# Performance work log

Measured on AMD Instinct MI355X. Metric: run time of the kernel, lower is better.

## Reference

```python
import jax, jax.numpy as jnp
import numpy as np

K = 0.001  # sigmoid temperature from DGCLoss init
EPS = 1e-8


def _off_diag(m):
    # [..., n, n] -> [..., n, n-1], removing the diagonal in row-major order
    n = m.shape[-1]
    lead = m.shape[:-2]
    flat = m.reshape(lead + (n * n,))[..., :-1]
    return flat.reshape(lead + (n - 1, n + 1))[..., 1:].reshape(lead + (n, n - 1))


def setup_inputs() -> dict:
    key = jax.random.key(0)
    k1, k2 = jax.random.split(key)
    ranking = jax.random.normal(k1, (384, 256), dtype=jnp.float32)
    gt = jax.random.randint(k2, (384,), 0, 6, dtype=jnp.int64)
    return {"ranking": ranking, "gt": gt}


def reference(ranking, gt):
    x = ranking
    N = x.shape[0]
    # cosine similarity matrix, mapped to [0, 1]
    xn = x / jnp.clip(jnp.linalg.norm(x, axis=1, keepdims=True), EPS, None)
    sm = (xn @ xn.T + 1.0) * 0.5                         # [N, N]
    rank = _off_diag(sm)                                 # [N, N-1]
    g = jnp.abs(gt[None, :] - gt[:, None]).astype(jnp.float32)  # [N, N]
    g = _off_diag(g)                                     # [N, N-1]
    M = N - 1
    # dij[n, i, j] = rank[n, j] - rank[n, i]
    dij = rank[:, None, :] - rank[:, :, None]            # [N, M, M]
    dij = _off_diag(dij)                                 # [N, M, M-1]
    # clamped sigmoid indicator
    indicator = 1.0 / (1.0 + jnp.exp(jnp.clip(-dij / K, -50.0, 50.0)))
    indicator = indicator.sum(-1) + 1.0                  # [N, M]
    relevance = jnp.exp2(jnp.clip(10.0 - g, 0.0, None)) - 1.0  # [N, M]
    dcg = (relevance / jnp.log2(indicator + 1.0)).sum(axis=1)  # [N]
    # ideal DCG from sorted relevance
    rel_sorted = jnp.sort(relevance, axis=-1)[:, ::-1]
    discount = jnp.log2(jnp.arange(M, dtype=jnp.float32) + 2.0)
    idcg = (rel_sorted / discount).sum(axis=-1)          # [N]
    valid = idcg != 0.0
    ndcg = jnp.where(valid, dcg / jnp.where(valid, idcg, 1.0), 0.0)
    cnt = valid.sum()
    mean_ndcg = ndcg.sum() / jnp.maximum(cnt, 1).astype(jnp.float32)
    return jnp.where(cnt == 0, jnp.float32(1.0), 1.0 - mean_ndcg)
```

## Files before the change

### kernel.cpp

```cpp
#include <hip/hip_runtime.h>


#define NN 384
#define DD 256
#define MM 383
#define HSCALE 721.3475204444817f
#define NBUCK  256
#define BSCALE 0.1767955801104972f
#define WWIN   6.0f

__global__ __launch_bounds__(256) void dgc_normT(const float* __restrict__ x,
                                                 const int* __restrict__ gt,
                                                 float* __restrict__ XT,
                                                 float* __restrict__ XN,
                                                 float* __restrict__ idcg_tab) {
    const int t = threadIdx.x;

    if (blockIdx.x == 24) {
        __shared__ int   cnt[6];
        __shared__ int   cum[6][6];
        __shared__ float wred[4][6];
        const int lane = t & 63;
        const int wave = t >> 6;

        if (t < 6) cnt[t] = 0;
        __syncthreads();
        atomicAdd(&cnt[gt[t]], 1);
        if (t + 256 < NN) atomicAdd(&cnt[gt[t + 256]], 1);
        __syncthreads();
        if (t < 6) {
            int h[6];
            #pragma unroll
            for (int g = 0; g < 6; ++g) h[g] = 0;
            #pragma unroll
            for (int v = 0; v < 6; ++v) {
                int d = v - t; d = d < 0 ? -d : d;
                h[d] += cnt[v];
            }
            h[0] -= 1;
            int s = 0;
            #pragma unroll
            for (int g = 0; g < 6; ++g) { s += h[g]; cum[t][g] = s; }
        }
        __syncthreads();

        float acc[6] = {0.f, 0.f, 0.f, 0.f, 0.f, 0.f};
        for (int p = t; p < MM; p += 256) {
            const float invl = 1.0f / __builtin_amdgcn_logf((float)(p + 2));
            #pragma unroll
            for (int gv = 0; gv < 6; ++gv) {
                const int g = (p >= cum[gv][0]) + (p >= cum[gv][1])
                            + (p >= cum[gv][2]) + (p >= cum[gv][3])
                            + (p >= cum[gv][4]);
                acc[gv] += (float)((1 << (10 - g)) - 1) * invl;
            }
        }
        for (int off = 32; off > 0; off >>= 1) {
            #pragma unroll
            for (int gv = 0; gv < 6; ++gv) acc[gv] += __shfl_down(acc[gv], off, 64);
        }
        if (lane == 0) {
            #pragma unroll
            for (int gv = 0; gv < 6; ++gv) wred[wave][gv] = acc[gv];
        }
        __syncthreads();
        if (t < 6) idcg_tab[t] = wred[0][t] + wred[1][t] + wred[2][t] + wred[3][t];
        return;
    }

    __shared__ float xs[16][260];
    __shared__ float invn[16];
    const int r0 = blockIdx.x * 16;

    #pragma unroll
    for (int i = 0; i < 4; ++i) {
        int f = t + i * 256;
        int r = f >> 6, c4 = f & 63;
        float4 v = ((const float4*)(x + (size_t)(r0 + r) * DD))[c4];
        xs[r][c4 * 4 + 0] = v.x; xs[r][c4 * 4 + 1] = v.y;
        xs[r][c4 * 4 + 2] = v.z; xs[r][c4 * 4 + 3] = v.w;
    }
    __syncthreads();

    {
        const int r = t >> 4, sub = t & 15;
        float s = 0.0f;
        #pragma unroll
        for (int m = 0; m < 16; ++m) {
            float v = xs[r][sub * 16 + m];
            s = fmaf(v, v, s);
        }
        #pragma unroll
        for (int off = 8; off > 0; off >>= 1) s += __shfl_xor(s, off, 64);
        if (sub == 0) invn[r] = __builtin_amdgcn_rsqf(fmaxf(s, 1e-16f));
    }
    __syncthreads();

    {
        const int r  = t & 15;
        const int kk = t >> 4;
        const float inv = invn[r];
        #pragma unroll
        for (int i = 0; i < 16; ++i) {
            int k = i * 16 + kk;
            XT[(size_t)k * NN + r0 + r] = xs[r][k] * inv;
        }
    }
    {
        #pragma unroll
        for (int i = 0; i < 4; ++i) {
            int f = t + i * 256;
            int r = f >> 6, c4 = f & 63;
            const float inv = invn[r];
            float4 v;
            v.x = xs[r][c4 * 4 + 0] * inv; v.y = xs[r][c4 * 4 + 1] * inv;
            v.z = xs[r][c4 * 4 + 2] * inv; v.w = xs[r][c4 * 4 + 3] * inv;
            ((float4*)(XN + (size_t)(r0 + r) * DD))[c4] = v;
        }
    }
}

__global__ __launch_bounds__(768) void dgc_fused(const float* __restrict__ XT,
                                                 const float* __restrict__ XN,
                                                 const int* __restrict__ gt,
                                                 const float* __restrict__ idcg_tab,
                                                 float* __restrict__ ndcg) {
    __shared__ float  xs[2][DD];
    __shared__ float4 pacc[2][8][96];
    __shared__ float  srow[2][NN];
    __shared__ float  vsort[2][NN];
    __shared__ int    sidx[2][NN];
    __shared__ int    hist[2][NBUCK];
    __shared__ int    pre[2][NBUCK + 1];
    __shared__ float  redd[12];

    const int n0   = blockIdx.x * 2;
    const int t    = threadIdx.x;
    const int lane = t & 63;
    const int wave = t >> 6;

    if (t < 128)
        ((float4*)xs[t >> 6])[t & 63] =
            ((const float4*)(XN + (size_t)(n0 + (t >> 6)) * DD))[t & 63];
    if (t < 512) ((int*)hist)[t] = 0;
    __syncthreads();

    {
        const int j4 = t % 96;
        const int kc = t / 96;
        const float4* XT4 = (const float4*)XT;
        float4 a0 = {0.f, 0.f, 0.f, 0.f};
        float4 a1 = {0.f, 0.f, 0.f, 0.f};
        const int k0 = kc * 32;
        #pragma unroll 8
        for (int m = 0; m < 32; ++m) {
            const int k = k0 + m;
            float4 b = XT4[(size_t)k * 96 + j4];
            float s0 = xs[0][k];
            float s1 = xs[1][k];
            a0.x = fmaf(s0, b.x, a0.x); a0.y = fmaf(s0, b.y, a0.y);
            a0.z = fmaf(s0, b.z, a0.z); a0.w = fmaf(s0, b.w, a0.w);
            a1.x = fmaf(s1, b.x, a1.x); a1.y = fmaf(s1, b.y, a1.y);
            a1.z = fmaf(s1, b.z, a1.z); a1.w = fmaf(s1, b.w, a1.w);
        }
        pacc[0][kc][j4] = a0;
        pacc[1][kc][j4] = a1;
    }
    __syncthreads();

    const int r = t / 384;
    const int u = t - r * 384;

    {
        const float* pf = (const float*)pacc[r];
        float dot = 0.0f;
        #pragma unroll
        for (int c = 0; c < 8; ++c) dot += pf[c * 384 + u];
        srow[r][u] = fmaf(dot, HSCALE, HSCALE);
    }
    __syncthreads();

    const float vraw = srow[r][u];
    int b = (int)(vraw * BSCALE);
    b = b < 0 ? 0 : (b > NBUCK - 1 ? NBUCK - 1 : b);
    const int slot = atomicAdd(&hist[r][b], 1);
    __syncthreads();

    if (wave == 0 || wave == 6) {
        const int rr = wave / 6;
        const int s0 = hist[rr][lane * 4 + 0], s1 = hist[rr][lane * 4 + 1];
        const int s2 = hist[rr][lane * 4 + 2], s3 = hist[rr][lane * 4 + 3];
        const int sum = s0 + s1 + s2 + s3;
        int inc = sum;
        #pragma unroll
        for (int off = 1; off < 64; off <<= 1) {
            int uu = __shfl_up(inc, off, 64);
            if (lane >= off) inc += uu;
        }
        const int base = inc - sum;
        pre[rr][lane * 4 + 0] = base;
        pre[rr][lane * 4 + 1] = base + s0;
        pre[rr][lane * 4 + 2] = base + s0 + s1;
        pre[rr][lane * 4 + 3] = base + s0 + s1 + s2;
        if (lane == 63) pre[rr][NBUCK] = inc;
    }
    __syncthreads();

    {
        const int pos = pre[r][b] + slot;
        vsort[r][pos] = vraw;
        sidx[r][pos]  = u;
    }
    __syncthreads();

    const int   nrow  = n0 + r;
    const float ri    = vsort[r][u];
    const int   iorig = sidx[r][u];
    const float sn    = srow[r][nrow];

    int Blo = (int)((ri - WWIN) * BSCALE);
    int Bhi = (int)((ri + WWIN) * BSCALE);
    Blo = Blo < 0 ? 0 : (Blo > NBUCK - 1 ? NBUCK - 1 : Blo);
    Bhi = Bhi < 0 ? 0 : (Bhi > NBUCK - 1 ? NBUCK - 1 : Bhi);
    const int lo = pre[r][Blo];
    const int hi = pre[r][Bhi + 1];

    float p0 = 0.0f, p1 = 0.0f;
    int q = lo;
    for (; q + 2 <= hi; q += 2) {
        p0 += __builtin_amdgcn_rcpf(1.0f + __builtin_amdgcn_exp2f(ri - vsort[r][q]));
        p1 += __builtin_amdgcn_rcpf(1.0f + __builtin_amdgcn_exp2f(ri - vsort[r][q + 1]));
    }
    if (q < hi)
        p0 += __builtin_amdgcn_rcpf(1.0f + __builtin_amdgcn_exp2f(ri - vsort[r][q]));
    float sum_all = (float)(NN - hi) + p0 + p1;

    int bn = (int)(sn * BSCALE);
    bn = bn < 0 ? 0 : (bn > NBUCK - 1 ? NBUCK - 1 : bn);
    float cd = 0.0f;
    if (bn > Bhi)       cd = 1.0f;
    else if (bn >= Blo) cd = __builtin_amdgcn_rcpf(1.0f + __builtin_amdgcn_exp2f(ri - sn));
    const float ind = 0.5f + sum_all - cd;

    float dcg_i = 0.0f;
    if (iorig != nrow) {
        const int gd = gt[iorig] - gt[nrow];
        const int gg = gd < 0 ? -gd : gd;
        dcg_i = (float)((1 << (10 - gg)) - 1) / __builtin_amdgcn_logf(ind + 1.0f);
    }

    #pragma unroll
    for (int off = 32; off > 0; off >>= 1) dcg_i += __shfl_down(dcg_i, off, 64);
    if (lane == 0) redd[wave] = dcg_i;
    __syncthreads();
    if (t == 0)
        ndcg[n0] = (redd[0] + redd[1] + redd[2] + redd[3] + redd[4] + redd[5])
                   / idcg_tab[gt[n0]];
    if (t == 384)
        ndcg[n0 + 1] = (redd[6] + redd[7] + redd[8] + redd[9] + redd[10] + redd[11])
                       / idcg_tab[gt[n0 + 1]];
}

__global__ __launch_bounds__(384) void dgc_final(const float* __restrict__ ndcg,
                                                 float* __restrict__ out) {
    __shared__ float red[6];
    const int t    = threadIdx.x;
    const int lane = t & 63;
    const int wave = t >> 6;
    float nd = ndcg[t];
    #pragma unroll
    for (int off = 32; off > 0; off >>= 1) nd += __shfl_down(nd, off, 64);
    if (lane == 0) red[wave] = nd;
    __syncthreads();
    if (t == 0) {
        float s = 0.0f;
        for (int w = 0; w < 6; ++w) s += red[w];
        out[0] = 1.0f - s / (float)NN;
    }
}

extern "C" void kernel_launch(void* const* d_in, const int* in_sizes, int n_in,
                              void* d_out, int out_size, void* d_ws, size_t ws_size,
                              hipStream_t stream) {
    const float* ranking = (const float*)d_in[0];
    const int*   gt      = (const int*)d_in[1];
    float*       out     = (float*)d_out;

    float* XT   = (float*)d_ws;
    float* XN   = XT + (size_t)DD * NN;
    float* ndcg = XN + (size_t)NN * DD;
    float* tab  = ndcg + NN;

    dgc_normT<<<25, 256, 0, stream>>>(ranking, gt, XT, XN, tab);
    dgc_fused<<<NN / 2, 768, 0, stream>>>(XT, XN, gt, tab, ndcg);
    dgc_final<<<1, 384, 0, stream>>>(ndcg, out);
}
```

Before: 70.10 us.

## Drop final reduction kernel via atomic accumulation and pair sigmoid reciprocals

Removes the third kernel launch. The output is initialised to 1 in the first kernel, and each fused block atomically subtracts its normalised DCG contribution directly. Separately, the windowed sigmoid sum now combines two terms per reciprocal using 1/(1+a)+1/(1+b) = (2+a+b)/(1+a+b+ab), which halves the rcp count. In exchange, the float atomics make the summation order nondeterministic, and the product form can overflow to inf when both exponentials are large.

```diff
diff --git a/kernel.cpp b/kernel.cpp
--- a/kernel.cpp
+++ b/kernel.cpp
@@ -13,7 +13,8 @@
                                                  const int* __restrict__ gt,
                                                  float* __restrict__ XT,
                                                  float* __restrict__ XN,
-                                                 float* __restrict__ idcg_tab) {
+                                                 float* __restrict__ idcg_tab,
+                                                 float* __restrict__ out) {
     const int t = threadIdx.x;
 
     if (blockIdx.x == 24) {
@@ -23,6 +24,7 @@
         const int lane = t & 63;
         const int wave = t >> 6;
 
+        if (t == 0) out[0] = 1.0f;
         if (t < 6) cnt[t] = 0;
         __syncthreads();
         atomicAdd(&cnt[gt[t]], 1);
@@ -124,7 +126,7 @@
                                                  const float* __restrict__ XN,
                                                  const int* __restrict__ gt,
                                                  const float* __restrict__ idcg_tab,
-                                                 float* __restrict__ ndcg) {
+                                                 float* __restrict__ out) {
     __shared__ float  xs[2][DD];
     __shared__ float4 pacc[2][8][96];
     __shared__ float  srow[2][NN];
@@ -225,15 +227,18 @@
     const int lo = pre[r][Blo];
     const int hi = pre[r][Bhi + 1];
 
-    float p0 = 0.0f, p1 = 0.0f;
+    float acc = 0.0f;
     int q = lo;
     for (; q + 2 <= hi; q += 2) {
-        p0 += __builtin_amdgcn_rcpf(1.0f + __builtin_amdgcn_exp2f(ri - vsort[r][q]));
-        p1 += __builtin_amdgcn_rcpf(1.0f + __builtin_amdgcn_exp2f(ri - vsort[r][q + 1]));
+        float a = __builtin_amdgcn_exp2f(ri - vsort[r][q]);
+        float bb = __builtin_amdgcn_exp2f(ri - vsort[r][q + 1]);
+        float e = a + bb;
+        float f = a * bb;
+        acc = fmaf(2.0f + e, __builtin_amdgcn_rcpf(1.0f + e + f), acc);
     }
     if (q < hi)
-        p0 += __builtin_amdgcn_rcpf(1.0f + __builtin_amdgcn_exp2f(ri - vsort[r][q]));
-    float sum_all = (float)(NN - hi) + p0 + p1;
+        acc += __builtin_amdgcn_rcpf(1.0f + __builtin_amdgcn_exp2f(ri - vsort[r][q]));
+    float sum_all = (float)(NN - hi) + acc;
 
     int bn = (int)(sn * BSCALE);
     bn = bn < 0 ? 0 : (bn > NBUCK - 1 ? NBUCK - 1 : bn);
@@ -253,29 +258,13 @@
     for (int off = 32; off > 0; off >>= 1) dcg_i += __shfl_down(dcg_i, off, 64);
     if (lane == 0) redd[wave] = dcg_i;
     __syncthreads();
-    if (t == 0)
-        ndcg[n0] = (redd[0] + redd[1] + redd[2] + redd[3] + redd[4] + redd[5])
-                   / idcg_tab[gt[n0]];
-    if (t == 384)
-        ndcg[n0 + 1] = (redd[6] + redd[7] + redd[8] + redd[9] + redd[10] + redd[11])
-                       / idcg_tab[gt[n0 + 1]];
-}
-
-__global__ __launch_bounds__(384) void dgc_final(const float* __restrict__ ndcg,
-                                                 float* __restrict__ out) {
-    __shared__ float red[6];
-    const int t    = threadIdx.x;
-    const int lane = t & 63;
-    const int wave = t >> 6;
-    float nd = ndcg[t];
-    #pragma unroll
-    for (int off = 32; off > 0; off >>= 1) nd += __shfl_down(nd, off, 64);
-    if (lane == 0) red[wave] = nd;
-    __syncthreads();
     if (t == 0) {
-        float s = 0.0f;
-        for (int w = 0; w < 6; ++w) s += red[w];
-        out[0] = 1.0f - s / (float)NN;
+        float d = redd[0] + redd[1] + redd[2] + redd[3] + redd[4] + redd[5];
+        atomicAdd(out, -d / (idcg_tab[gt[n0]] * (float)NN));
+    }
+    if (t == 384) {
+        float d = redd[6] + redd[7] + redd[8] + redd[9] + redd[10] + redd[11];
+        atomicAdd(out, -d / (idcg_tab[gt[n0 + 1]] * (float)NN));
     }
 }
 
@@ -286,12 +275,10 @@
     const int*   gt      = (const int*)d_in[1];
     float*       out     = (float*)d_out;
 
-    float* XT   = (float*)d_ws;
-    float* XN   = XT + (size_t)DD * NN;
-    float* ndcg = XN + (size_t)NN * DD;
-    float* tab  = ndcg + NN;
-
-    dgc_normT<<<25, 256, 0, stream>>>(ranking, gt, XT, XN, tab);
-    dgc_fused<<<NN / 2, 768, 0, stream>>>(XT, XN, gt, tab, ndcg);
-    dgc_final<<<1, 384, 0, stream>>>(ndcg, out);
+    float* XT  = (float*)d_ws;
+    float* XN  = XT + (size_t)DD * NN;
+    float* tab = XN + (size_t)NN * DD;
+
+    dgc_normT<<<25, 256, 0, stream>>>(ranking, gt, XT, XN, tab, out);
+    dgc_fused<<<NN / 2, 768, 0, stream>>>(XT, XN, gt, tab, out);
 }
```

New measurement: 74.10 us. 5.7% more time.
